# Kernel optimization log

Measured on AMD Instinct MI355X. Metric: run time of the kernel, lower is better.

Reference implementation:

```python
import jax, jax.numpy as jnp
import numpy as np

E = 2.718281828459045  # math.e
B, A, N = 128, 512, 256


def setup_inputs() -> dict:
    key = jax.random.key(0)
    k1, k2, k3 = jax.random.split(key, 3)
    # atomic numbers: positive integers (1..89) stored as float32
    atomic_numbers = jax.random.randint(k1, (B, A), 1, 90).astype(jnp.float32)
    # neighbor indices into the atom axis [0, A)
    neighbors = jax.random.randint(k2, (B, A, N), 0, A).astype(jnp.int32)
    # pairwise distances, positive
    r_ij = jax.random.uniform(k3, (B, A, N), dtype=jnp.float32) * 5.0 + 0.5
    return {"atomic_numbers": atomic_numbers, "neighbors": neighbors, "r_ij": r_ij}


def reference(atomic_numbers, neighbors, r_ij):
    # a_i: [B, A, 1] central-atom atomic numbers
    a_i = atomic_numbers[:, :, None]
    # gather neighbor atomic numbers: out[b,i,j] = atomic_numbers[b, neighbors[b,i,j]]
    a_j = jax.vmap(lambda an, nb: an[nb])(atomic_numbers, neighbors)  # [B, A, N]
    # fused elementwise edit: exp(-0.05*e * (a_i*a_j)^1.01 / (a_i+a_j)^1.1)
    dist_edit = jnp.exp(-0.05 * E * jnp.power(a_i * a_j, 1.01)
                        / jnp.power(a_i + a_j, 1.1))
    return r_ij + dist_edit
```

## Files before the change

kernel.cpp:

```cpp
#include <hip/hip_runtime.h>


#define BB 128
#define AA 512
#define NN 256
#define ROWS 64
#define TPB 256

__global__ __launch_bounds__(TPB, 4) void RAN_72567767433723_kernel(
    const float* __restrict__ an,
    const int*   __restrict__ nbrs,
    const float* __restrict__ rij,
    float*       __restrict__ out)
{
    __shared__ float tab[90 * 90];
    __shared__ int   zrow[AA];

    const int tid = threadIdx.x;
    const int bid = blockIdx.x;
    const int b        = bid >> 3;
    const int row_base = (bid & 7) * ROWS;

    for (int i = tid; i < AA; i += TPB)
        zrow[i] = (int)(an[b * AA + i] + 0.5f);

    const float c = -0.05f * 2.718281828459045f;
    for (int idx = tid; idx < 90 * 90; idx += TPB) {
        int zi = idx / 90;
        int zj = idx - zi * 90;
        float p = fmaxf((float)(zi * zj), 1.0f);
        float s = fmaxf((float)(zi + zj), 1.0f);
        tab[idx] = __expf(c * __powf(p, 1.01f) / __powf(s, 1.1f));
    }
    __syncthreads();

    const int lane_row = tid >> 6;
    const int c4       = tid & 63;

    #pragma unroll 4
    for (int it = 0; it < ROWS / 4; ++it) {
        const int a      = row_base + it * 4 + lane_row;
        const int tbase  = zrow[a] * 90;
        const size_t e   = ((size_t)(b * AA + a) * NN) + (size_t)c4 * 4;

        const int4   nb = *(const int4*)(nbrs + e);
        const float4 r  = *(const float4*)(rij + e);

        float4 o;
        o.x = r.x + tab[tbase + zrow[nb.x]];
        o.y = r.y + tab[tbase + zrow[nb.y]];
        o.z = r.z + tab[tbase + zrow[nb.z]];
        o.w = r.w + tab[tbase + zrow[nb.w]];

        *(float4*)(out + e) = o;
    }
}

extern "C" void kernel_launch(void* const* d_in, const int* in_sizes, int n_in,
                              void* d_out, int out_size, void* d_ws, size_t ws_size,
                              hipStream_t stream) {
    const float* an  = (const float*)d_in[0];
    const int*   nbr = (const int*)d_in[1];
    const float* rij = (const float*)d_in[2];
    float*       o   = (float*)d_out;

    const int grid = (BB * AA) / ROWS;
    RAN_72567767433723_kernel<<<grid, TPB, 0, stream>>>(an, nbr, rij, o);
}
```

Measured before the change: 203.7 us.

## Precompute fp16 lookup table once in workspace and copy into LDS per block

Builds the pairwise exp/pow table once per call in a separate kernel in workspace memory as fp16, and each block copies it into shared memory with vector loads instead of recomputing transcendental functions. Rows per block are halved, occupancy hint raised, atomic numbers stored as ushort, and streaming loads/stores marked nontemporal. Risks fp16 rounding of the table values and an extra kernel launch.

```diff
diff --git a/kernel.cpp b/kernel.cpp
--- a/kernel.cpp
+++ b/kernel.cpp
@@ -4,55 +4,75 @@
 #define BB 128
 #define AA 512
 #define NN 256
-#define ROWS 64
+#define ROWS 32
 #define TPB 256
+#define TABN 8192
 
-__global__ __launch_bounds__(TPB, 4) void RAN_72567767433723_kernel(
+typedef int   v4i __attribute__((ext_vector_type(4)));
+typedef float v4f __attribute__((ext_vector_type(4)));
+
+__device__ __forceinline__ float tab_entry(int idx) {
+    int zi = idx / 90, zj = idx - zi * 90;
+    float p = fmaxf((float)(zi * zj), 1.0f);
+    float s = fmaxf((float)(zi + zj), 1.0f);
+    const float c = -0.05f * 2.718281828459045f;
+    return __expf(c * __powf(p, 1.01f) / __powf(s, 1.1f));
+}
+
+__global__ void RAN_72567767433723_build_tab(_Float16* __restrict__ tabg) {
+    int idx = blockIdx.x * blockDim.x + threadIdx.x;
+    tabg[idx] = (_Float16)tab_entry(idx);
+}
+
+template <bool LOAD_TAB>
+__global__ __launch_bounds__(TPB, 8) void RAN_72567767433723_kernel(
     const float* __restrict__ an,
     const int*   __restrict__ nbrs,
     const float* __restrict__ rij,
-    float*       __restrict__ out)
+    float*       __restrict__ out,
+    const _Float16* __restrict__ tabg)
 {
-    __shared__ float tab[90 * 90];
-    __shared__ int   zrow[AA];
+    __shared__ _Float16       tab[TABN];
+    __shared__ unsigned short zz[AA];
 
-    const int tid = threadIdx.x;
-    const int bid = blockIdx.x;
-    const int b        = bid >> 3;
-    const int row_base = (bid & 7) * ROWS;
+    const int tid      = threadIdx.x;
+    const int b        = blockIdx.x >> 4;
+    const int row_base = (blockIdx.x & 15) * ROWS;
 
+    if (LOAD_TAB) {
+        #pragma unroll
+        for (int i = 0; i < TABN * 2 / (16 * TPB); ++i) {
+            int k = i * TPB + tid;
+            ((v4i*)tab)[k] = ((const v4i*)tabg)[k];
+        }
+    } else {
+        for (int idx = tid; idx < TABN; idx += TPB)
+            tab[idx] = (_Float16)tab_entry(idx);
+    }
+    #pragma unroll
     for (int i = tid; i < AA; i += TPB)
-        zrow[i] = (int)(an[b * AA + i] + 0.5f);
-
-    const float c = -0.05f * 2.718281828459045f;
-    for (int idx = tid; idx < 90 * 90; idx += TPB) {
-        int zi = idx / 90;
-        int zj = idx - zi * 90;
-        float p = fmaxf((float)(zi * zj), 1.0f);
-        float s = fmaxf((float)(zi + zj), 1.0f);
-        tab[idx] = __expf(c * __powf(p, 1.01f) / __powf(s, 1.1f));
-    }
+        zz[i] = (unsigned short)(int)(an[b * AA + i] + 0.5f);
     __syncthreads();
 
-    const int lane_row = tid >> 6;
-    const int c4       = tid & 63;
+    const int w = tid >> 6;
+    const int l = tid & 63;
 
-    #pragma unroll 4
+    #pragma unroll 2
     for (int it = 0; it < ROWS / 4; ++it) {
-        const int a      = row_base + it * 4 + lane_row;
-        const int tbase  = zrow[a] * 90;
-        const size_t e   = ((size_t)(b * AA + a) * NN) + (size_t)c4 * 4;
+        const int a     = row_base + it * 4 + w;
+        const int tb    = (int)zz[a] * 90;
+        const size_t e  = ((size_t)(b * AA + a)) * NN + (size_t)(l * 4);
 
-        const int4   nb = *(const int4*)(nbrs + e);
-        const float4 r  = *(const float4*)(rij + e);
+        const v4i nb = __builtin_nontemporal_load((const v4i*)(nbrs + e));
+        const v4f r  = __builtin_nontemporal_load((const v4f*)(rij + e));
 
-        float4 o;
-        o.x = r.x + tab[tbase + zrow[nb.x]];
-        o.y = r.y + tab[tbase + zrow[nb.y]];
-        o.z = r.z + tab[tbase + zrow[nb.z]];
-        o.w = r.w + tab[tbase + zrow[nb.w]];
+        v4f o;
+        o.x = r.x + (float)tab[tb + (int)zz[nb.x]];
+        o.y = r.y + (float)tab[tb + (int)zz[nb.y]];
+        o.z = r.z + (float)tab[tb + (int)zz[nb.z]];
+        o.w = r.w + (float)tab[tb + (int)zz[nb.w]];
 
-        *(float4*)(out + e) = o;
+        __builtin_nontemporal_store(o, (v4f*)(out + e));
     }
 }
 
@@ -65,5 +85,12 @@
     float*       o   = (float*)d_out;
 
     const int grid = (BB * AA) / ROWS;
-    RAN_72567767433723_kernel<<<grid, TPB, 0, stream>>>(an, nbr, rij, o);
+
+    if (ws_size >= (size_t)TABN * sizeof(_Float16)) {
+        _Float16* tabg = (_Float16*)d_ws;
+        RAN_72567767433723_build_tab<<<TABN / TPB, TPB, 0, stream>>>(tabg);
+        RAN_72567767433723_kernel<true><<<grid, TPB, 0, stream>>>(an, nbr, rij, o, tabg);
+    } else {
+        RAN_72567767433723_kernel<false><<<grid, TPB, 0, stream>>>(an, nbr, rij, o, nullptr);
+    }
 }
```

New measurement: 167.0 us. 1.22x faster.
